# Optimization experiments

Measured on AMD Instinct MI355X. Metric: run time of the kernel, lower is better.

## Reference

```python
import jax, jax.numpy as jnp
import numpy as np


def setup_inputs() -> dict:
    key = jax.random.key(0)
    ks = jax.random.split(key, 5)
    b, t, e, h = 8, 1024, 256, 8
    w = lambda k, shape: jax.random.normal(k, shape, dtype=jnp.float32) * 0.02
    return {
        "x": jax.random.normal(ks[0], (b, t, e), dtype=jnp.float32),
        "Wq": w(ks[1], (e, e * h)), "bq": jnp.zeros((e * h,), jnp.float32),
        "Wk": w(ks[2], (e, e * h)), "bk": jnp.zeros((e * h,), jnp.float32),
        "Wv": w(ks[3], (e, e * h)), "bv": jnp.zeros((e * h,), jnp.float32),
        "Wu": w(ks[4], (e * h, e)), "bu": jnp.zeros((e,), jnp.float32),
    }


def reference(x, Wq, bq, Wk, bk, Wv, bv, Wu, bu):
    b, t, e = x.shape
    h = Wq.shape[1] // e  # each head has FULL width e in this module
    q = (x @ Wq + bq).reshape(b, t, h, e)
    k = (x @ Wk + bk).reshape(b, t, h, e)
    v = (x @ Wv + bv).reshape(b, t, h, e)
    # scores: (b, h, t, t), scaled by sqrt(e) as in the original
    scores = jnp.einsum('bihe,bjhe->bhij', q, k) / jnp.sqrt(jnp.asarray(e, jnp.float32))
    i = jnp.arange(t)[:, None]
    j = jnp.arange(t)[None, :]
    # mask mode 'first': triu(offset=0) -> -inf, i.e. query i sees only j < i
    scores = jnp.where(j >= i, -jnp.inf, scores)
    # row 0 is fully masked (torch softmax -> NaN, then zeroed post-softmax);
    # make it finite first so softmax is well-defined, then zero the attention row
    scores = jnp.where(i == 0, 0.0, scores)
    att = jax.nn.softmax(scores, axis=-1)
    att = jnp.where(i == 0, 0.0, att)
    out = jnp.einsum('bhij,bjhe->bihe', att, v).reshape(b, t, h * e)
    return out @ Wu + bu
```

## Files before the change

kernel.cpp:

```cpp
#include <hip/hip_runtime.h>
#include <hip/hip_bf16.h>

typedef unsigned short u16;
typedef short bf16x8 __attribute__((ext_vector_type(8)));
typedef float f32x4 __attribute__((ext_vector_type(4)));

#define EXP2(x) __builtin_amdgcn_exp2f(x)

static __device__ __forceinline__ u16 f2bf(float f) {
  union { float f; unsigned u; } a; a.f = f;
  unsigned r = a.u + 0x7fffu + ((a.u >> 16) & 1u);
  return (u16)(r >> 16);
}

static __device__ __forceinline__ unsigned pkbf(float a, float b) {
  union { __hip_bfloat162 h; unsigned u; } c;
  c.h = __float22bfloat162_rn(make_float2(a, b));
  return c.u;
}

static __device__ __forceinline__ bf16x8 as_bf(int4 v) {
  union { int4 i; bf16x8 b; } u; u.i = v; return u.b;
}

#define GLDS16(g, l)                                         \
  __builtin_amdgcn_global_load_lds(                          \
      (const __attribute__((address_space(1))) void*)(g),    \
      (__attribute__((address_space(3))) void*)(l), 16, 0, 0)

__global__ __launch_bounds__(256) void prep(
    const float* __restrict__ x, u16* __restrict__ Xb,
    const float* __restrict__ Wq, u16* __restrict__ Wqt,
    const float* __restrict__ Wk, u16* __restrict__ Wkt,
    const float* __restrict__ Wv, u16* __restrict__ Wvt,
    const float* __restrict__ Wu, u16* __restrict__ Wut) {
  const int bid = blockIdx.x, tid = threadIdx.x;
  if (bid < 1024) {
    int i = bid * 256 + tid;
    const float4* p = (const float4*)x + (size_t)i * 2;
    float4 a = p[0], b = p[1];
    union { unsigned s[4]; int4 v; } u2;
    u2.s[0] = pkbf(a.x, a.y); u2.s[1] = pkbf(a.z, a.w);
    u2.s[2] = pkbf(b.x, b.y); u2.s[3] = pkbf(b.z, b.w);
    ((int4*)Xb)[i] = u2.v;
    return;
  }
  const int which = (bid - 1024) >> 6;
  const float* in; u16* out; int R, C;
  if (which == 0)      { in = Wq; out = Wqt; R = 256;  C = 2048; }
  else if (which == 1) { in = Wk; out = Wkt; R = 256;  C = 2048; }
  else if (which == 2) { in = Wv; out = Wvt; R = 256;  C = 2048; }
  else                 { in = Wu; out = Wut; R = 2048; C = 256;  }
  int T = ((bid - 1024) & 63) * 256 + tid;
  int c = T % C;
  int r0 = (T / C) * 32;
  __align__(16) u16 tmp[32];
#pragma unroll
  for (int j = 0; j < 32; ++j) tmp[j] = f2bf(in[(size_t)(r0 + j) * C + c]);
#pragma unroll
  for (int q = 0; q < 4; ++q)
    *(int4*)(out + (size_t)c * R + r0 + q * 8) = *(int4*)&tmp[q * 8];
}

__global__ __launch_bounds__(256) void gemm_qkv(const u16* __restrict__ A,
                                                const u16* __restrict__ Wt,
                                                const float* __restrict__ bq,
                                                const float* __restrict__ bk,
                                                const float* __restrict__ bv,
                                                u16* __restrict__ Qw,
                                                u16* __restrict__ Kw,
                                                u16* __restrict__ Vt) {
  constexpr int BM = 128, BN = 128, BK = 64;
  __shared__ int4 smem4[2048];
  int4* As4 = smem4;
  int4* Bs4 = smem4 + 1024;
  const int tid = threadIdx.x;
  const int w = tid >> 6, lane = tid & 63, lq = lane & 15, quad = lane >> 4;
  const int wm = w >> 1, wn = w & 1;
  const int m0 = blockIdx.y * BM, n0 = blockIdx.x * BN;
  const int z = blockIdx.z;

  const u16* Btz = Wt + (size_t)z * 2048 * 256;
  const float* bias = (z == 0) ? bq : (z == 1 ? bk : bv);

  const int srow = lane >> 3;
  const int scb = (lane & 7) ^ ((lane >> 3) & 7);

  f32x4 acc[4][4];
#pragma unroll
  for (int mi = 0; mi < 4; ++mi)
#pragma unroll
    for (int ni = 0; ni < 4; ++ni) {
      f32x4 z4 = {0.f, 0.f, 0.f, 0.f};
      acc[mi][ni] = z4;
    }

  for (int k0 = 0; k0 < 256; k0 += BK) {
    __syncthreads();
#pragma unroll
    for (int it = 0; it < 4; ++it) {
      int r = (w * 4 + it) * 8 + srow;
      GLDS16(A + (size_t)(m0 + r) * 256 + k0 + scb * 8,
             (char*)As4 + (w * 4 + it) * 1024);
    }
#pragma unroll
    for (int it = 0; it < 4; ++it) {
      int r = (w * 4 + it) * 8 + srow;
      GLDS16(Btz + (size_t)(n0 + r) * 256 + k0 + scb * 8,
             (char*)Bs4 + (w * 4 + it) * 1024);
    }
    __syncthreads();
#pragma unroll
    for (int kk = 0; kk < 2; ++kk) {
      int4 af[4], bf[4];
#pragma unroll
      for (int mi = 0; mi < 4; ++mi) {
        int r = wm * 64 + mi * 16 + lq;
        af[mi] = As4[r * 8 + ((kk * 4 + quad) ^ (lq & 7))];
      }
#pragma unroll
      for (int ni = 0; ni < 4; ++ni) {
        int r = wn * 64 + ni * 16 + lq;
        bf[ni] = Bs4[r * 8 + ((kk * 4 + quad) ^ (lq & 7))];
      }
#pragma unroll
      for (int mi = 0; mi < 4; ++mi)
#pragma unroll
        for (int ni = 0; ni < 4; ++ni)
          acc[mi][ni] = __builtin_amdgcn_mfma_f32_16x16x32_bf16(
              as_bf(af[mi]), as_bf(bf[ni]), acc[mi][ni], 0, 0, 0);
    }
  }

  if (z < 2) {
    u16* Cout = z ? Kw : Qw;
#pragma unroll
    for (int mi = 0; mi < 4; ++mi)
#pragma unroll
      for (int ni = 0; ni < 4; ++ni)
#pragma unroll
        for (int r = 0; r < 4; ++r) {
          int row = m0 + wm * 64 + mi * 16 + quad * 4 + r;
          int col = n0 + wn * 64 + ni * 16 + lq;
          Cout[(size_t)row * 2048 + col] = f2bf(acc[mi][ni][r] + bias[col]);
        }
  } else {
    __syncthreads();
    u16* Ts = (u16*)smem4;
#pragma unroll
    for (int mi = 0; mi < 4; ++mi)
#pragma unroll
      for (int ni = 0; ni < 4; ++ni) {
        int c = wn * 64 + ni * 16 + lq;
        int r0 = wm * 64 + mi * 16 + quad * 4;
        float vb = bias[n0 + c];
        uint2 dd;
        dd.x = pkbf(acc[mi][ni][0] + vb, acc[mi][ni][1] + vb);
        dd.y = pkbf(acc[mi][ni][2] + vb, acc[mi][ni][3] + vb);
        *(uint2*)&Ts[c * 128 + (((r0 >> 3) ^ (c & 15)) << 3) + (r0 & 7)] = dd;
      }
    __syncthreads();
    const int b = m0 >> 10, t0 = m0 & 1023;
    const int e0 = n0 & 255, h = n0 >> 8;
    const int bh = b * 8 + h;
    const int i4 = tid & 15;
#pragma unroll
    for (int cc = 0; cc < 8; ++cc) {
      int c = (tid >> 4) + cc * 16;
      int4 val = *(const int4*)&Ts[c * 128 + ((i4 ^ (c & 15)) << 3)];
      *(int4*)(Vt + (size_t)(bh * 256 + e0 + c) * 1024 + t0 + i4 * 8) = val;
    }
  }
}

template <int BM, int BN>
__global__ __launch_bounds__(256) void gemm_bt(const u16* __restrict__ A,
                                               const u16* __restrict__ Bt,
                                               const float* __restrict__ bias,
                                               float* __restrict__ Cout,
                                               int M, int N, int K) {
  constexpr int BK = 64;
  constexpr int TM = BM / 2 / 16, TN = BN / 2 / 16;
  constexpr int nA = BM / 32, nB = BN / 32;
  __shared__ int4 As4[BM * 8];
  __shared__ int4 Bs4[BN * 8];
  const int tid = threadIdx.x;
  const int w = tid >> 6, lane = tid & 63, lq = lane & 15, quad = lane >> 4;
  const int wm = w >> 1, wn = w & 1;
  const int m0 = blockIdx.y * BM, n0 = blockIdx.x * BN;

  const int srow = lane >> 3;
  const int scb = (lane & 7) ^ ((lane >> 3) & 7);

  f32x4 acc[TM][TN];
#pragma unroll
  for (int mi = 0; mi < TM; ++mi)
#pragma unroll
    for (int ni = 0; ni < TN; ++ni) {
      f32x4 z4 = {0.f, 0.f, 0.f, 0.f};
      acc[mi][ni] = z4;
    }

  for (int k0 = 0; k0 < K; k0 += BK) {
    __syncthreads();
#pragma unroll
    for (int it = 0; it < nA; ++it) {
      int r = (w * nA + it) * 8 + srow;
      GLDS16(A + (size_t)(m0 + r) * K + k0 + scb * 8,
             (char*)As4 + (w * nA + it) * 1024);
    }
#pragma unroll
    for (int it = 0; it < nB; ++it) {
      int r = (w * nB + it) * 8 + srow;
      GLDS16(Bt + (size_t)(n0 + r) * K + k0 + scb * 8,
             (char*)Bs4 + (w * nB + it) * 1024);
    }
    __syncthreads();
#pragma unroll
    for (int kk = 0; kk < BK / 32; ++kk) {
      int4 af[TM], bf[TN];
#pragma unroll
      for (int mi = 0; mi < TM; ++mi) {
        int r = wm * (BM / 2) + mi * 16 + lq;
        af[mi] = As4[r * 8 + ((kk * 4 + quad) ^ (lq & 7))];
      }
#pragma unroll
      for (int ni = 0; ni < TN; ++ni) {
        int r = wn * (BN / 2) + ni * 16 + lq;
        bf[ni] = Bs4[r * 8 + ((kk * 4 + quad) ^ (lq & 7))];
      }
#pragma unroll
      for (int mi = 0; mi < TM; ++mi)
#pragma unroll
        for (int ni = 0; ni < TN; ++ni)
          acc[mi][ni] = __builtin_amdgcn_mfma_f32_16x16x32_bf16(
              as_bf(af[mi]), as_bf(bf[ni]), acc[mi][ni], 0, 0, 0);
    }
  }

#pragma unroll
  for (int mi = 0; mi < TM; ++mi)
#pragma unroll
    for (int ni = 0; ni < TN; ++ni)
#pragma unroll
      for (int r = 0; r < 4; ++r) {
        int row = m0 + wm * (BM / 2) + mi * 16 + quad * 4 + r;
        int col = n0 + wn * (BN / 2) + ni * 16 + lq;
        Cout[(size_t)row * N + col] = acc[mi][ni][r] + bias[col];
      }
}

__global__ __launch_bounds__(256, 2) void attn_kernel(const u16* __restrict__ Q,
                                                      const u16* __restrict__ Km,
                                                      const u16* __restrict__ Vt,
                                                      u16* __restrict__ O) {
  const int bh = blockIdx.x;
  const int pair = blockIdx.y;
  const int b = bh >> 3, h = bh & 7;
  const int tid = threadIdx.x;
  const int w = tid >> 6, lane = tid & 63, lq = lane & 15, quad = lane >> 4;

  __shared__ int4 Ks4[2048];
  __shared__ int4 Vs4[2048];
  __shared__ u16 Ps[4096];
  u16* myPs = Ps + w * 1024;

  int koffb[8], voffb[8];
  {
    const int kg = (lane & 31) >> 3;
#pragma unroll
    for (int it = 0; it < 8; ++it) {
      int r = w * 16 + it * 2 + (lane >> 5);
      int p = (lane & 7) ^ (r & 7);
      koffb[it] = r * 2048 + (kg * 8 + p) * 8;
      int rv = w * 64 + it * 8 + (lane >> 3);
      int cb = (lane & 7) ^ (rv & 7);
      voffb[it] = rv * 1024 + cb * 8;
    }
  }
  const u16* kbase = Km + (size_t)b * 2097152 + h * 256;
  const u16* vbase = Vt + (size_t)bh * 262144;

  const float SCL = 0.09016844f;
  const float NEG = -3.0e38f;

#pragma unroll 1
  for (int hv = 0; hv < 2; ++hv) {
    const int qt = hv ? (15 - pair) : pair;
    const int qg = qt * 64 + w * 16 + lq;
    const u16* qptr = Q + (size_t)(b * 1024 + qg) * 2048 + h * 256 + quad * 8;
    int4 qf[8];
#pragma unroll
    for (int kk = 0; kk < 8; ++kk) qf[kk] = *(const int4*)(qptr + kk * 32);

    f32x4 of[16];
#pragma unroll
    for (int i = 0; i < 16; ++i) {
      f32x4 z = {0.f, 0.f, 0.f, 0.f};
      of[i] = z;
    }
    float mst = NEG, lst = 0.f;

    for (int kt = 0; kt <= qt; ++kt) {
      __syncthreads();
      {
        const u16* kb = kbase + (size_t)kt * 131072;
        const u16* vb = vbase + kt * 64;
#pragma unroll
        for (int it = 0; it < 8; ++it)
          GLDS16(kb + koffb[it], (char*)Ks4 + (w * 8 + it) * 1024);
#pragma unroll
        for (int it = 0; it < 8; ++it)
          GLDS16(vb + voffb[it], (char*)Vs4 + (w * 8 + it) * 1024);
      }
      __syncthreads();

      f32x4 sc[4];
#pragma unroll
      for (int ns = 0; ns < 4; ++ns) {
        f32x4 a = {0.f, 0.f, 0.f, 0.f};
        int r = ns * 16 + lq;
#pragma unroll
        for (int kk = 0; kk < 8; ++kk) {
          int G = kk * 4 + quad;
          int4 kf = Ks4[r * 32 + (G >> 3) * 8 + ((G & 7) ^ (lq & 7))];
          a = __builtin_amdgcn_mfma_f32_16x16x32_bf16(as_bf(kf), as_bf(qf[kk]),
                                                      a, 0, 0, 0);
        }
        sc[ns] = a;
      }
#pragma unroll
      for (int ns = 0; ns < 4; ++ns) {
        int keyb = kt * 64 + ns * 16 + quad * 4;
#pragma unroll
        for (int r = 0; r < 4; ++r) {
          float v = sc[ns][r] * SCL;
          sc[ns][r] = (keyb + r >= qg) ? NEG : v;
        }
      }
      float m16 = sc[0][0];
#pragma unroll
      for (int ns = 0; ns < 4; ++ns)
#pragma unroll
        for (int r = 0; r < 4; ++r) m16 = fmaxf(m16, sc[ns][r]);
      m16 = fmaxf(m16, __shfl_xor(m16, 16));
      m16 = fmaxf(m16, __shfl_xor(m16, 32));
      if (__any(m16 > mst)) {
        float mn = fmaxf(mst, m16);
        float alpha = EXP2(mst - mn);
        mst = mn;
        lst *= alpha;
#pragma unroll
        for (int i = 0; i < 16; ++i)
#pragma unroll
          for (int r = 0; r < 4; ++r) of[i][r] *= alpha;
      }
      float s = 0.f;
#pragma unroll
      for (int ns = 0; ns < 4; ++ns)
#pragma unroll
        for (int r = 0; r < 4; ++r) {
          float p = EXP2(sc[ns][r] - mst);
          sc[ns][r] = p;
          s += p;
        }
      s += __shfl_xor(s, 16);
      s += __shfl_xor(s, 32);
      lst += s;

#pragma unroll
      for (int ns = 0; ns < 4; ++ns) {
        int kb2 = ns * 2 + (quad >> 1);
        int base = lq * 64 + ((kb2 ^ (lq & 7)) << 3) + (quad & 1) * 4;
        *(unsigned*)&myPs[base] = pkbf(sc[ns][0], sc[ns][1]);
        *(unsigned*)&myPs[base + 2] = pkbf(sc[ns][2], sc[ns][3]);
      }
      int4 pf[2];
#pragma unroll
      for (int kk2 = 0; kk2 < 2; ++kk2) {
        int kbp = (kk2 * 4 + quad) ^ (lq & 7);
        pf[kk2] = *(const int4*)&myPs[lq * 64 + kbp * 8];
      }
#pragma unroll
      for (int ns2 = 0; ns2 < 16; ++ns2) {
        int r = ns2 * 16 + lq;
#pragma unroll
        for (int kk2 = 0; kk2 < 2; ++kk2) {
          int4 vf = Vs4[r * 8 + ((kk2 * 4 + quad) ^ (lq & 7))];
          of[ns2] = __builtin_amdgcn_mfma_f32_16x16x32_bf16(
              as_bf(vf), as_bf(pf[kk2]), of[ns2], 0, 0, 0);
        }
      }
    }

    float inv = lst > 0.f ? 1.f / lst : 0.f;
    if (qg == 0) inv = 0.f;
    u16* optr = O + (size_t)(b * 1024 + qg) * 2048 + h * 256 + quad * 4;
#pragma unroll
    for (int ns2 = 0; ns2 < 16; ++ns2) {
      uint2 o4;
      o4.x = pkbf(of[ns2][0] * inv, of[ns2][1] * inv);
      o4.y = pkbf(of[ns2][2] * inv, of[ns2][3] * inv);
      *(uint2*)(optr + ns2 * 16) = o4;
    }
  }
}

#define WS_XB 0
#define WS_WQT 4194304
#define WS_WUT 7340032
#define WS_QW 8388608
#define WS_KW 41943040
#define WS_OW 75497472
#define WS_VTW 109051904

extern "C" void kernel_launch(void* const* d_in, const int* in_sizes, int n_in,
                              void* d_out, int out_size, void* d_ws, size_t ws_size,
                              hipStream_t stream) {
  const float* x = (const float*)d_in[0];
  const float* Wq = (const float*)d_in[1];
  const float* bq = (const float*)d_in[2];
  const float* Wk = (const float*)d_in[3];
  const float* bk = (const float*)d_in[4];
  const float* Wv = (const float*)d_in[5];
  const float* bv = (const float*)d_in[6];
  const float* Wu = (const float*)d_in[7];
  const float* bu = (const float*)d_in[8];
  float* out = (float*)d_out;

  char* ws = (char*)d_ws;
  u16* Xb = (u16*)(ws + WS_XB);
  u16* Wqt = (u16*)(ws + WS_WQT);
  u16* Wkt = Wqt + 524288;
  u16* Wvt = Wqt + 1048576;
  u16* Wut = (u16*)(ws + WS_WUT);
  u16* Qw = (u16*)(ws + WS_QW);
  u16* Kw = (u16*)(ws + WS_KW);
  u16* Ow = (u16*)(ws + WS_OW);
  u16* Vtw = (u16*)(ws + WS_VTW);

  prep<<<1280, 256, 0, stream>>>(x, Xb, Wq, Wqt, Wk, Wkt, Wv, Wvt, Wu, Wut);

  gemm_qkv<<<dim3(16, 64, 3), 256, 0, stream>>>(Xb, Wqt, bq, bk, bv, Qw, Kw, Vtw);

  attn_kernel<<<dim3(64, 8), 256, 0, stream>>>(Qw, Kw, Vtw, Ow);

  gemm_bt<128, 64><<<dim3(4, 64), 256, 0, stream>>>(Ow, Wut, bu, out, 8192, 256, 2048);
}
```

Before: 220.0 us.

## Double-buffer K/V tiles and share them across two query tiles per block

The attention kernel now runs 512 threads (8 waves). The two wave groups process a mirrored pair of query tiles that share each staged K/V tile, so loads are amortized across twice the queries. K/V staging is double-buffered, with the next tile's load issued before computing the current one. This removes one barrier per iteration and hides global-to-LDS latency. It also adds s_setprio around the MFMA sections. In exchange, LDS use doubles (K/V plus P buffers), and the grid halves, which may reduce occupancy.

```diff
diff --git a/kernel.cpp b/kernel.cpp
--- a/kernel.cpp
+++ b/kernel.cpp
@@ -250,30 +250,31 @@
       }
 }
 
-__global__ __launch_bounds__(256, 2) void attn_kernel(const u16* __restrict__ Q,
+__global__ __launch_bounds__(512, 2) void attn_kernel(const u16* __restrict__ Q,
                                                       const u16* __restrict__ Km,
                                                       const u16* __restrict__ Vt,
                                                       u16* __restrict__ O) {
   const int bh = blockIdx.x;
-  const int pair = blockIdx.y;
   const int b = bh >> 3, h = bh & 7;
   const int tid = threadIdx.x;
   const int w = tid >> 6, lane = tid & 63, lq = lane & 15, quad = lane >> 4;
-
-  __shared__ int4 Ks4[2048];
-  __shared__ int4 Vs4[2048];
-  __shared__ u16 Ps[4096];
+  const int wl = w & 3;
+  const int tg = w >> 2;
+
+  __shared__ int4 KV[8192];
+  __shared__ u16 Ps[8192];
   u16* myPs = Ps + w * 1024;
 
-  int koffb[8], voffb[8];
+  int koffb[4], voffb[4];
   {
     const int kg = (lane & 31) >> 3;
 #pragma unroll
-    for (int it = 0; it < 8; ++it) {
-      int r = w * 16 + it * 2 + (lane >> 5);
-      int p = (lane & 7) ^ (r & 7);
-      koffb[it] = r * 2048 + (kg * 8 + p) * 8;
-      int rv = w * 64 + it * 8 + (lane >> 3);
+    for (int it = 0; it < 4; ++it) {
+      int j = w * 4 + it;
+      int r = j * 2 + (lane >> 5);
+      int pz = (lane & 7) ^ (r & 7);
+      koffb[it] = r * 2048 + (kg * 8 + pz) * 8;
+      int rv = j * 8 + (lane >> 3);
       int cb = (lane & 7) ^ (rv & 7);
       voffb[it] = rv * 1024 + cb * 8;
     }
@@ -281,13 +282,28 @@
   const u16* kbase = Km + (size_t)b * 2097152 + h * 256;
   const u16* vbase = Vt + (size_t)bh * 262144;
 
+  auto STAGE = [&](int bufsel, int kt) {
+    const u16* kb = kbase + (size_t)kt * 131072;
+    const u16* vb = vbase + kt * 64;
+    char* kd = (char*)(KV + bufsel * 4096);
+    char* vd = (char*)(KV + bufsel * 4096 + 2048);
+#pragma unroll
+    for (int it = 0; it < 4; ++it)
+      GLDS16(kb + koffb[it], kd + (w * 4 + it) * 1024);
+#pragma unroll
+    for (int it = 0; it < 4; ++it)
+      GLDS16(vb + voffb[it], vd + (w * 4 + it) * 1024);
+  };
+
   const float SCL = 0.09016844f;
   const float NEG = -3.0e38f;
 
 #pragma unroll 1
-  for (int hv = 0; hv < 2; ++hv) {
-    const int qt = hv ? (15 - pair) : pair;
-    const int qg = qt * 64 + w * 16 + lq;
+  for (int pass = 0; pass < 2; ++pass) {
+    const int pp = pass ? (7 - (int)blockIdx.y) : (int)blockIdx.y;
+    const int qt = tg ? pp : (15 - pp);
+    const int kmax = 15 - pp;
+    const int qg = qt * 64 + wl * 16 + lq;
     const u16* qptr = Q + (size_t)(b * 1024 + qg) * 2048 + h * 256 + quad * 8;
     int4 qf[8];
 #pragma unroll
@@ -301,96 +317,101 @@
     }
     float mst = NEG, lst = 0.f;
 
-    for (int kt = 0; kt <= qt; ++kt) {
+    int buf = 0;
+    STAGE(0, 0);
+    __syncthreads();
+
+    for (int kt = 0; kt <= kmax; ++kt) {
+      if (kt < kmax) STAGE(buf ^ 1, kt + 1);
+
+      if (kt <= qt) {
+        const int4* Kc = KV + buf * 4096;
+        const int4* Vc = Kc + 2048;
+
+        f32x4 sc[4];
+        __builtin_amdgcn_s_setprio(1);
+#pragma unroll
+        for (int ns = 0; ns < 4; ++ns) {
+          f32x4 a = {0.f, 0.f, 0.f, 0.f};
+          int r = ns * 16 + lq;
+#pragma unroll
+          for (int kk = 0; kk < 8; ++kk) {
+            int G = kk * 4 + quad;
+            int4 kf = Kc[r * 32 + (G >> 3) * 8 + ((G & 7) ^ (lq & 7))];
+            a = __builtin_amdgcn_mfma_f32_16x16x32_bf16(as_bf(kf), as_bf(qf[kk]),
+                                                        a, 0, 0, 0);
+          }
+          sc[ns] = a;
+        }
+        __builtin_amdgcn_s_setprio(0);
+#pragma unroll
+        for (int ns = 0; ns < 4; ++ns) {
+          int keyb = kt * 64 + ns * 16 + quad * 4;
+#pragma unroll
+          for (int r = 0; r < 4; ++r) {
+            float v = sc[ns][r] * SCL;
+            sc[ns][r] = (keyb + r >= qg) ? NEG : v;
+          }
+        }
+        float m16 = sc[0][0];
+#pragma unroll
+        for (int ns = 0; ns < 4; ++ns)
+#pragma unroll
+          for (int r = 0; r < 4; ++r) m16 = fmaxf(m16, sc[ns][r]);
+        m16 = fmaxf(m16, __shfl_xor(m16, 16));
+        m16 = fmaxf(m16, __shfl_xor(m16, 32));
+        if (__any(m16 > mst)) {
+          float mn = fmaxf(mst, m16);
+          float alpha = EXP2(mst - mn);
+          mst = mn;
+          lst *= alpha;
+#pragma unroll
+          for (int i = 0; i < 16; ++i)
+#pragma unroll
+            for (int r = 0; r < 4; ++r) of[i][r] *= alpha;
+        }
+        float s = 0.f;
+#pragma unroll
+        for (int ns = 0; ns < 4; ++ns)
+#pragma unroll
+          for (int r = 0; r < 4; ++r) {
+            float p = EXP2(sc[ns][r] - mst);
+            sc[ns][r] = p;
+            s += p;
+          }
+        s += __shfl_xor(s, 16);
+        s += __shfl_xor(s, 32);
+        lst += s;
+
+#pragma unroll
+        for (int ns = 0; ns < 4; ++ns) {
+          int kb2 = ns * 2 + (quad >> 1);
+          int base = lq * 64 + ((kb2 ^ (lq & 7)) << 3) + (quad & 1) * 4;
+          *(unsigned*)&myPs[base] = pkbf(sc[ns][0], sc[ns][1]);
+          *(unsigned*)&myPs[base + 2] = pkbf(sc[ns][2], sc[ns][3]);
+        }
+        int4 pf[2];
+#pragma unroll
+        for (int kk2 = 0; kk2 < 2; ++kk2) {
+          int kbp = (kk2 * 4 + quad) ^ (lq & 7);
+          pf[kk2] = *(const int4*)&myPs[lq * 64 + kbp * 8];
+        }
+        __builtin_amdgcn_s_setprio(1);
+#pragma unroll
+        for (int ns2 = 0; ns2 < 16; ++ns2) {
+          int r = ns2 * 16 + lq;
+#pragma unroll
+          for (int kk2 = 0; kk2 < 2; ++kk2) {
+            int4 vf = Vc[r * 8 + ((kk2 * 4 + quad) ^ (lq & 7))];
+            of[ns2] = __builtin_amdgcn_mfma_f32_16x16x32_bf16(
+                as_bf(vf), as_bf(pf[kk2]), of[ns2], 0, 0, 0);
+          }
+        }
+        __builtin_amdgcn_s_setprio(0);
+      }
+
       __syncthreads();
-      {
-        const u16* kb = kbase + (size_t)kt * 131072;
-        const u16* vb = vbase + kt * 64;
-#pragma unroll
-        for (int it = 0; it < 8; ++it)
-          GLDS16(kb + koffb[it], (char*)Ks4 + (w * 8 + it) * 1024);
-#pragma unroll
-        for (int it = 0; it < 8; ++it)
-          GLDS16(vb + voffb[it], (char*)Vs4 + (w * 8 + it) * 1024);
-      }
-      __syncthreads();
-
-      f32x4 sc[4];
-#pragma unroll
-      for (int ns = 0; ns < 4; ++ns) {
-        f32x4 a = {0.f, 0.f, 0.f, 0.f};
-        int r = ns * 16 + lq;
-#pragma unroll
-        for (int kk = 0; kk < 8; ++kk) {
-          int G = kk * 4 + quad;
-          int4 kf = Ks4[r * 32 + (G >> 3) * 8 + ((G & 7) ^ (lq & 7))];
-          a = __builtin_amdgcn_mfma_f32_16x16x32_bf16(as_bf(kf), as_bf(qf[kk]),
-                                                      a, 0, 0, 0);
-        }
-        sc[ns] = a;
-      }
-#pragma unroll
-      for (int ns = 0; ns < 4; ++ns) {
-        int keyb = kt * 64 + ns * 16 + quad * 4;
-#pragma unroll
-        for (int r = 0; r < 4; ++r) {
-          float v = sc[ns][r] * SCL;
-          sc[ns][r] = (keyb + r >= qg) ? NEG : v;
-        }
-      }
-      float m16 = sc[0][0];
-#pragma unroll
-      for (int ns = 0; ns < 4; ++ns)
-#pragma unroll
-        for (int r = 0; r < 4; ++r) m16 = fmaxf(m16, sc[ns][r]);
-      m16 = fmaxf(m16, __shfl_xor(m16, 16));
-      m16 = fmaxf(m16, __shfl_xor(m16, 32));
-      if (__any(m16 > mst)) {
-        float mn = fmaxf(mst, m16);
-        float alpha = EXP2(mst - mn);
-        mst = mn;
-        lst *= alpha;
-#pragma unroll
-        for (int i = 0; i < 16; ++i)
-#pragma unroll
-          for (int r = 0; r < 4; ++r) of[i][r] *= alpha;
-      }
-      float s = 0.f;
-#pragma unroll
-      for (int ns = 0; ns < 4; ++ns)
-#pragma unroll
-        for (int r = 0; r < 4; ++r) {
-          float p = EXP2(sc[ns][r] - mst);
-          sc[ns][r] = p;
-          s += p;
-        }
-      s += __shfl_xor(s, 16);
-      s += __shfl_xor(s, 32);
-      lst += s;
-
-#pragma unroll
-      for (int ns = 0; ns < 4; ++ns) {
-        int kb2 = ns * 2 + (quad >> 1);
-        int base = lq * 64 + ((kb2 ^ (lq & 7)) << 3) + (quad & 1) * 4;
-        *(unsigned*)&myPs[base] = pkbf(sc[ns][0], sc[ns][1]);
-        *(unsigned*)&myPs[base + 2] = pkbf(sc[ns][2], sc[ns][3]);
-      }
-      int4 pf[2];
-#pragma unroll
-      for (int kk2 = 0; kk2 < 2; ++kk2) {
-        int kbp = (kk2 * 4 + quad) ^ (lq & 7);
-        pf[kk2] = *(const int4*)&myPs[lq * 64 + kbp * 8];
-      }
-#pragma unroll
-      for (int ns2 = 0; ns2 < 16; ++ns2) {
-        int r = ns2 * 16 + lq;
-#pragma unroll
-        for (int kk2 = 0; kk2 < 2; ++kk2) {
-          int4 vf = Vs4[r * 8 + ((kk2 * 4 + quad) ^ (lq & 7))];
-          of[ns2] = __builtin_amdgcn_mfma_f32_16x16x32_bf16(
-              as_bf(vf), as_bf(pf[kk2]), of[ns2], 0, 0, 0);
-        }
-      }
+      buf ^= 1;
     }
 
     float inv = lst > 0.f ? 1.f / lst : 0.f;
@@ -443,7 +464,7 @@
 
   gemm_qkv<<<dim3(16, 64, 3), 256, 0, stream>>>(Xb, Wqt, bq, bk, bv, Qw, Kw, Vtw);
 
-  attn_kernel<<<dim3(64, 8), 256, 0, stream>>>(Qw, Kw, Vtw, Ow);
+  attn_kernel<<<dim3(64, 4), 512, 0, stream>>>(Qw, Kw, Vtw, Ow);
 
   gemm_bt<128, 64><<<dim3(4, 64), 256, 0, stream>>>(Ow, Wut, bu, out, 8192, 256, 2048);
 }
```

New measurement: 230.4 us. 1.05x slower.

## Process 128-query tiles per block with two 16-row query sets per wave

Applied to the files above, without the earlier changes.

Each block now handles one 128-row query tile instead of two paired 64-row tiles. Each wave holds two 16-row query fragments, so every K/V fragment read from shared memory feeds two MFMAs, and each K/V tile is loaded once for twice as many queries. Blocks are mapped through a 1D grid with heavy and light tiles interleaved, and s_setprio is raised around the MFMA sections. The cost is twice the accumulator registers per wave. Waves whose rows end earlier sit idle on the final key tile, which unbalances work within a block.

```diff
diff --git a/kernel.cpp b/kernel.cpp
--- a/kernel.cpp
+++ b/kernel.cpp
@@ -254,8 +254,10 @@
                                                       const u16* __restrict__ Km,
                                                       const u16* __restrict__ Vt,
                                                       u16* __restrict__ O) {
-  const int bh = blockIdx.x;
-  const int pair = blockIdx.y;
+  const int bid = blockIdx.x;
+  const int bh = bid & 63;
+  const int g = bid >> 6;
+  const int s = (g < 4) ? g : (11 - g);
   const int b = bh >> 3, h = bh & 7;
   const int tid = threadIdx.x;
   const int w = tid >> 6, lane = tid & 63, lq = lane & 15, quad = lane >> 4;
@@ -284,125 +286,196 @@
   const float SCL = 0.09016844f;
   const float NEG = -3.0e38f;
 
-#pragma unroll 1
-  for (int hv = 0; hv < 2; ++hv) {
-    const int qt = hv ? (15 - pair) : pair;
-    const int qg = qt * 64 + w * 16 + lq;
-    const u16* qptr = Q + (size_t)(b * 1024 + qg) * 2048 + h * 256 + quad * 8;
-    int4 qf[8];
-#pragma unroll
-    for (int kk = 0; kk < 8; ++kk) qf[kk] = *(const int4*)(qptr + kk * 32);
-
-    f32x4 of[16];
-#pragma unroll
-    for (int i = 0; i < 16; ++i) {
-      f32x4 z = {0.f, 0.f, 0.f, 0.f};
-      of[i] = z;
-    }
-    float mst = NEG, lst = 0.f;
-
-    for (int kt = 0; kt <= qt; ++kt) {
-      __syncthreads();
-      {
-        const u16* kb = kbase + (size_t)kt * 131072;
-        const u16* vb = vbase + kt * 64;
-#pragma unroll
-        for (int it = 0; it < 8; ++it)
-          GLDS16(kb + koffb[it], (char*)Ks4 + (w * 8 + it) * 1024);
-#pragma unroll
-        for (int it = 0; it < 8; ++it)
-          GLDS16(vb + voffb[it], (char*)Vs4 + (w * 8 + it) * 1024);
-      }
-      __syncthreads();
-
-      f32x4 sc[4];
+  const int kmax = 2 * s + 1;
+  const int wkt = 2 * s + (w >> 1);
+  const int qgA = s * 128 + w * 32 + lq;
+
+  const u16* qpA = Q + (size_t)(b * 1024 + qgA) * 2048 + h * 256 + quad * 8;
+  int4 qa[8], qb[8];
+#pragma unroll
+  for (int kk = 0; kk < 8; ++kk) {
+    qa[kk] = *(const int4*)(qpA + kk * 32);
+    qb[kk] = *(const int4*)(qpA + 16 * 2048 + kk * 32);
+  }
+
+  f32x4 ofA[16], ofB[16];
+#pragma unroll
+  for (int i = 0; i < 16; ++i) {
+    f32x4 z = {0.f, 0.f, 0.f, 0.f};
+    ofA[i] = z;
+    ofB[i] = z;
+  }
+  float mA = NEG, lA = 0.f, mB = NEG, lB = 0.f;
+
+  for (int kt = 0; kt <= kmax; ++kt) {
+    __syncthreads();
+    {
+      const u16* kb = kbase + (size_t)kt * 131072;
+      const u16* vb = vbase + kt * 64;
+#pragma unroll
+      for (int it = 0; it < 8; ++it)
+        GLDS16(kb + koffb[it], (char*)Ks4 + (w * 8 + it) * 1024);
+#pragma unroll
+      for (int it = 0; it < 8; ++it)
+        GLDS16(vb + voffb[it], (char*)Vs4 + (w * 8 + it) * 1024);
+    }
+    __syncthreads();
+
+    if (kt <= wkt) {
+      f32x4 sA[4], sB[4];
+      __builtin_amdgcn_s_setprio(1);
 #pragma unroll
       for (int ns = 0; ns < 4; ++ns) {
-        f32x4 a = {0.f, 0.f, 0.f, 0.f};
+        f32x4 aA = {0.f, 0.f, 0.f, 0.f}, aB = {0.f, 0.f, 0.f, 0.f};
         int r = ns * 16 + lq;
 #pragma unroll
         for (int kk = 0; kk < 8; ++kk) {
           int G = kk * 4 + quad;
           int4 kf = Ks4[r * 32 + (G >> 3) * 8 + ((G & 7) ^ (lq & 7))];
-          a = __builtin_amdgcn_mfma_f32_16x16x32_bf16(as_bf(kf), as_bf(qf[kk]),
-                                                      a, 0, 0, 0);
+          aA = __builtin_amdgcn_mfma_f32_16x16x32_bf16(as_bf(kf), as_bf(qa[kk]),
+                                                       aA, 0, 0, 0);
+          aB = __builtin_amdgcn_mfma_f32_16x16x32_bf16(as_bf(kf), as_bf(qb[kk]),
+                                                       aB, 0, 0, 0);
         }
-        sc[ns] = a;
-      }
+        sA[ns] = aA;
+        sB[ns] = aB;
+      }
+      __builtin_amdgcn_s_setprio(0);
 #pragma unroll
       for (int ns = 0; ns < 4; ++ns) {
         int keyb = kt * 64 + ns * 16 + quad * 4;
 #pragma unroll
         for (int r = 0; r < 4; ++r) {
-          float v = sc[ns][r] * SCL;
-          sc[ns][r] = (keyb + r >= qg) ? NEG : v;
+          float vA = sA[ns][r] * SCL;
+          float vB = sB[ns][r] * SCL;
+          sA[ns][r] = (keyb + r >= qgA) ? NEG : vA;
+          sB[ns][r] = (keyb + r >= qgA + 16) ? NEG : vB;
         }
       }
-      float m16 = sc[0][0];
-#pragma unroll
-      for (int ns = 0; ns < 4; ++ns)
-#pragma unroll
-        for (int r = 0; r < 4; ++r) m16 = fmaxf(m16, sc[ns][r]);
-      m16 = fmaxf(m16, __shfl_xor(m16, 16));
-      m16 = fmaxf(m16, __shfl_xor(m16, 32));
-      if (__any(m16 > mst)) {
-        float mn = fmaxf(mst, m16);
-        float alpha = EXP2(mst - mn);
-        mst = mn;
-        lst *= alpha;
-#pragma unroll
-        for (int i = 0; i < 16; ++i)
-#pragma unroll
-          for (int r = 0; r < 4; ++r) of[i][r] *= alpha;
-      }
-      float s = 0.f;
-#pragma unroll
-      for (int ns = 0; ns < 4; ++ns)
-#pragma unroll
-        for (int r = 0; r < 4; ++r) {
-          float p = EXP2(sc[ns][r] - mst);
-          sc[ns][r] = p;
-          s += p;
+      {
+        float m16 = sA[0][0];
+#pragma unroll
+        for (int ns = 0; ns < 4; ++ns)
+#pragma unroll
+          for (int r = 0; r < 4; ++r) m16 = fmaxf(m16, sA[ns][r]);
+        m16 = fmaxf(m16, __shfl_xor(m16, 16));
+        m16 = fmaxf(m16, __shfl_xor(m16, 32));
+        if (__any(m16 > mA)) {
+          float mn = fmaxf(mA, m16);
+          float alpha = EXP2(mA - mn);
+          mA = mn;
+          lA *= alpha;
+#pragma unroll
+          for (int i = 0; i < 16; ++i)
+#pragma unroll
+            for (int r = 0; r < 4; ++r) ofA[i][r] *= alpha;
         }
-      s += __shfl_xor(s, 16);
-      s += __shfl_xor(s, 32);
-      lst += s;
-
+        float sum = 0.f;
+#pragma unroll
+        for (int ns = 0; ns < 4; ++ns)
+#pragma unroll
+          for (int r = 0; r < 4; ++r) {
+            float p = EXP2(sA[ns][r] - mA);
+            sA[ns][r] = p;
+            sum += p;
+          }
+        sum += __shfl_xor(sum, 16);
+        sum += __shfl_xor(sum, 32);
+        lA += sum;
+      }
+      {
+        float m16 = sB[0][0];
+#pragma unroll
+        for (int ns = 0; ns < 4; ++ns)
+#pragma unroll
+          for (int r = 0; r < 4; ++r) m16 = fmaxf(m16, sB[ns][r]);
+        m16 = fmaxf(m16, __shfl_xor(m16, 16));
+        m16 = fmaxf(m16, __shfl_xor(m16, 32));
+        if (__any(m16 > mB)) {
+          float mn = fmaxf(mB, m16);
+          float alpha = EXP2(mB - mn);
+          mB = mn;
+          lB *= alpha;
+#pragma unroll
+          for (int i = 0; i < 16; ++i)
+#pragma unroll
+            for (int r = 0; r < 4; ++r) ofB[i][r] *= alpha;
+        }
+        float sum = 0.f;
+#pragma unroll
+        for (int ns = 0; ns < 4; ++ns)
+#pragma unroll
+          for (int r = 0; r < 4; ++r) {
+            float p = EXP2(sB[ns][r] - mB);
+            sB[ns][r] = p;
+            sum += p;
+          }
+        sum += __shfl_xor(sum, 16);
+        sum += __shfl_xor(sum, 32);
+        lB += sum;
+      }
+
+      int4 pfA[2], pfB[2];
 #pragma unroll
       for (int ns = 0; ns < 4; ++ns) {
         int kb2 = ns * 2 + (quad >> 1);
         int base = lq * 64 + ((kb2 ^ (lq & 7)) << 3) + (quad & 1) * 4;
-        *(unsigned*)&myPs[base] = pkbf(sc[ns][0], sc[ns][1]);
-        *(unsigned*)&myPs[base + 2] = pkbf(sc[ns][2], sc[ns][3]);
-      }
-      int4 pf[2];
+        uint2 dd;
+        dd.x = pkbf(sA[ns][0], sA[ns][1]);
+        dd.y = pkbf(sA[ns][2], sA[ns][3]);
+        *(uint2*)&myPs[base] = dd;
+      }
 #pragma unroll
       for (int kk2 = 0; kk2 < 2; ++kk2) {
         int kbp = (kk2 * 4 + quad) ^ (lq & 7);
-        pf[kk2] = *(const int4*)&myPs[lq * 64 + kbp * 8];
-      }
+        pfA[kk2] = *(const int4*)&myPs[lq * 64 + kbp * 8];
+      }
+#pragma unroll
+      for (int ns = 0; ns < 4; ++ns) {
+        int kb2 = ns * 2 + (quad >> 1);
+        int base = lq * 64 + ((kb2 ^ (lq & 7)) << 3) + (quad & 1) * 4;
+        uint2 dd;
+        dd.x = pkbf(sB[ns][0], sB[ns][1]);
+        dd.y = pkbf(sB[ns][2], sB[ns][3]);
+        *(uint2*)&myPs[base] = dd;
+      }
+#pragma unroll
+      for (int kk2 = 0; kk2 < 2; ++kk2) {
+        int kbp = (kk2 * 4 + quad) ^ (lq & 7);
+        pfB[kk2] = *(const int4*)&myPs[lq * 64 + kbp * 8];
+      }
+
+      __builtin_amdgcn_s_setprio(1);
 #pragma unroll
       for (int ns2 = 0; ns2 < 16; ++ns2) {
         int r = ns2 * 16 + lq;
 #pragma unroll
         for (int kk2 = 0; kk2 < 2; ++kk2) {
           int4 vf = Vs4[r * 8 + ((kk2 * 4 + quad) ^ (lq & 7))];
-          of[ns2] = __builtin_amdgcn_mfma_f32_16x16x32_bf16(
-              as_bf(vf), as_bf(pf[kk2]), of[ns2], 0, 0, 0);
+          ofA[ns2] = __builtin_amdgcn_mfma_f32_16x16x32_bf16(
+              as_bf(vf), as_bf(pfA[kk2]), ofA[ns2], 0, 0, 0);
+          ofB[ns2] = __builtin_amdgcn_mfma_f32_16x16x32_bf16(
+              as_bf(vf), as_bf(pfB[kk2]), ofB[ns2], 0, 0, 0);
         }
       }
-    }
-
-    float inv = lst > 0.f ? 1.f / lst : 0.f;
-    if (qg == 0) inv = 0.f;
-    u16* optr = O + (size_t)(b * 1024 + qg) * 2048 + h * 256 + quad * 4;
-#pragma unroll
-    for (int ns2 = 0; ns2 < 16; ++ns2) {
-      uint2 o4;
-      o4.x = pkbf(of[ns2][0] * inv, of[ns2][1] * inv);
-      o4.y = pkbf(of[ns2][2] * inv, of[ns2][3] * inv);
-      *(uint2*)(optr + ns2 * 16) = o4;
-    }
+      __builtin_amdgcn_s_setprio(0);
+    }
+  }
+
+  float invA = lA > 0.f ? 1.f / lA : 0.f;
+  if (qgA == 0) invA = 0.f;
+  float invB = lB > 0.f ? 1.f / lB : 0.f;
+  u16* opA = O + (size_t)(b * 1024 + qgA) * 2048 + h * 256 + quad * 4;
+  u16* opB = opA + 16 * 2048;
+#pragma unroll
+  for (int ns2 = 0; ns2 < 16; ++ns2) {
+    uint2 oa, ob;
+    oa.x = pkbf(ofA[ns2][0] * invA, ofA[ns2][1] * invA);
+    oa.y = pkbf(ofA[ns2][2] * invA, ofA[ns2][3] * invA);
+    ob.x = pkbf(ofB[ns2][0] * invB, ofB[ns2][1] * invB);
+    ob.y = pkbf(ofB[ns2][2] * invB, ofB[ns2][3] * invB);
+    *(uint2*)(opA + ns2 * 16) = oa;
+    *(uint2*)(opB + ns2 * 16) = ob;
   }
 }
 
@@ -443,7 +516,7 @@
 
   gemm_qkv<<<dim3(16, 64, 3), 256, 0, stream>>>(Xb, Wqt, bq, bk, bv, Qw, Kw, Vtw);
 
-  attn_kernel<<<dim3(64, 8), 256, 0, stream>>>(Qw, Kw, Vtw, Ow);
+  attn_kernel<<<dim3(512), 256, 0, stream>>>(Qw, Kw, Vtw, Ow);
 
   gemm_bt<128, 64><<<dim3(4, 64), 256, 0, stream>>>(Ow, Wut, bu, out, 8192, 256, 2048);
 }
```

New measurement: 258.0 us. 17.3% more time.
